# Kernel optimization log

Measured on AMD Instinct MI355X. Metric: run time of the kernel, lower is better.

## Reference

```python
import jax, jax.numpy as jnp
import numpy as np
import math


def _forward(x, f0, theta, sigma, theta0, fbs, mix, w1, b1, w2, b2, conv_w):
    B, I, H, W = x.shape          # config requires B == I == H (== W here)
    S, O, _ = f0.shape            # config requires O == 1
    # ---- log-Gabor filter bank, fully vectorized over (scale, out, in) ----
    yy = jnp.linspace(-1.0, 1.0, H)[:, None]   # meshgrid 'ij': y along rows
    xx = jnp.linspace(-1.0, 1.0, W)[None, :]
    r = jnp.sqrt(xx ** 2 + yy ** 2 + 1e-6)     # [H,W]
    phi = jnp.arctan2(yy, xx)                  # [H,W]
    lr = jnp.log(r)
    log_gabor = jnp.exp(-(lr - jnp.log(f0)[..., None, None]) ** 2
                        / (2.0 * jnp.log(sigma)[..., None, None] ** 2))
    angular = jnp.exp(-(phi - theta[..., None, None]) ** 2
                      / (2.0 * theta0[..., None, None] ** 2))
    filters = log_gabor * angular              # [S,O,I,H,W]
    # ---- FFT (torch fftshift default shifts ALL dims; jnp matches) ----
    xs = jnp.fft.fftshift(jnp.fft.fft2(x))     # [B,I,H,W] complex64
    # ---- frequency attention (two 1x1 convs + softmax over scales) ----
    h1 = jax.nn.relu(jnp.einsum('bchw,oc->bohw', jnp.abs(xs), w1)
                     + b1[None, :, None, None])
    aw = jax.nn.softmax(jnp.einsum('bchw,sc->bshw', h1, w2)
                        + b2[None, :, None, None], axis=1)   # [B,S,H,W]
    # ---- attention-weighted combine. Faithful to torch broadcasting with
    # O==1 and B==I: attended[0,b,i,h,w] = sum_s xs[b,i]*F[s,0,i]*aw[i,s] ----
    attended = jnp.einsum('bihw,sihw,ishw->bihw', xs, filters[:, 0], aw)[None]
    # ---- dynamic frequency band mask (torch slices dims 2,3 = (Cin,H)) ----
    s_idx = jnp.floor((fbs[0, :, 0] + 1.0) / 2.0 * H).astype(jnp.int32)  # [I]
    e_idx = jnp.floor((fbs[0, :, 1] + 1.0) / 2.0 * H).astype(jnp.int32)
    arI = jnp.arange(I)
    arH = jnp.arange(H)
    mk = (arI[None, :] >= s_idx[:, None]) & (arI[None, :] < e_idx[:, None])  # [J,I]
    mh = (arH[None, :] >= s_idx[:, None]) & (arH[None, :] < e_idx[:, None])  # [J,H]
    mask = (mk[:, :, None] & mh[:, None, :]).astype(x.dtype)                 # [J,I,H]
    attended = attended * mask[None, :, :, :, None]
    # ---- back to spatial domain ----
    x_filtered = jnp.fft.ifft2(jnp.fft.ifftshift(attended)).real  # [1,B,I,H,W]
    # ---- spatial 3x3 conv path ----
    x_spatial = jax.lax.conv_general_dilated(
        x, conv_w, window_strides=(1, 1), padding=((1, 1), (1, 1)),
        dimension_numbers=('NCHW', 'OIHW', 'NCHW'))               # [B,1,H,W]
    return mix * x_filtered + (1.0 - mix) * x_spatial[None]


def setup_inputs() -> dict:
    key = jax.random.key(0)
    ks = jax.random.split(key, 10)
    B = I = H = W = 64
    O, S, HID = 1, 3, 64
    PI = math.pi
    x = jax.random.normal(ks[0], (B, I, H, W), dtype=jnp.float32)
    f0 = jnp.ones((S, O, I), jnp.float32)
    theta0 = jnp.ones((S, O, I), jnp.float32)
    sigma = jax.random.uniform(ks[1], (S, O, I), jnp.float32) * PI
    theta = jax.random.uniform(ks[2], (S, O, I), jnp.float32) * PI
    fbs = jax.random.uniform(ks[3], (O, I, 2), jnp.float32)
    mix = jax.random.uniform(ks[4], (1,), jnp.float32)
    w1 = jax.random.normal(ks[5], (HID, I), jnp.float32) * 0.05
    b1 = jnp.zeros((HID,), jnp.float32)
    w2 = jax.random.normal(ks[6], (S, HID), jnp.float32) * 0.05
    b2 = jnp.zeros((S,), jnp.float32)
    conv_w = jax.random.normal(ks[7], (O, I, 3, 3), jnp.float32) / math.sqrt(I * 9)
    return {'x': x, 'f0': f0, 'theta': theta, 'sigma': sigma, 'theta0': theta0,
            'fbs': fbs, 'mix': mix, 'w1': w1, 'b1': b1, 'w2': w2, 'b2': b2,
            'conv_w': conv_w}


def reference(x, f0, theta, sigma, theta0, fbs, mix, w1, b1, w2, b2, conv_w):
    return _forward(x, f0, theta, sigma, theta0, fbs, mix, w1, b1, w2, b2, conv_w)
```

## Files before the change

kernel.cpp:

```cpp
#include <hip/hip_runtime.h>

#define PI_D 3.14159265358979323846

namespace {
constexpr float CT[33] = {
  1.0000000000f,  0.9951847267f,  0.9807852804f,  0.9569403357f,
  0.9238795325f,  0.8819212643f,  0.8314696123f,  0.7730104534f,
  0.7071067812f,  0.6343932842f,  0.5555702330f,  0.4713967368f,
  0.3826834324f,  0.2902846773f,  0.1950903220f,  0.0980171403f,
  0.0f,          -0.0980171403f, -0.1950903220f, -0.2902846773f,
 -0.3826834324f, -0.4713967368f, -0.5555702330f, -0.6343932842f,
 -0.7071067812f, -0.7730104534f, -0.8314696123f, -0.8819212643f,
 -0.9238795325f, -0.9569403357f, -0.9807852804f, -0.9951847267f,
 -1.0f};
constexpr float STb[33] = {
  0.0f,           0.0980171403f,  0.1950903220f,  0.2902846773f,
  0.3826834324f,  0.4713967368f,  0.5555702330f,  0.6343932842f,
  0.7071067812f,  0.7730104534f,  0.8314696123f,  0.8819212643f,
  0.9238795325f,  0.9569403357f,  0.9807852804f,  0.9951847267f,
  1.0f,           0.9951847267f,  0.9807852804f,  0.9569403357f,
  0.9238795325f,  0.8819212643f,  0.8314696123f,  0.7730104534f,
  0.7071067812f,  0.6343932842f,  0.5555702330f,  0.4713967368f,
  0.3826834324f,  0.2902846773f,  0.1950903220f,  0.0980171403f,
  0.0f};
}

__device__ __forceinline__ void bitrev64(float v[64]) {
#pragma unroll
  for (int i = 0; i < 64; ++i) {
    const int j = (int)(__brev((unsigned)i) >> 26);
    if (j > i) { const float tv = v[i]; v[i] = v[j]; v[j] = tv; }
  }
}

template <bool INV, bool REAL>
__device__ __forceinline__ void fft64_stages(float re[64], float im[64]) {
#pragma unroll
  for (int s = 0; s < 6; ++s) {
    const int half = 1 << s;
    const int m = half << 1;
    const int tstep = 32 >> s;
#pragma unroll
    for (int k = 0; k < 64; k += m) {
#pragma unroll
      for (int j = 0; j < half; ++j) {
        const int ti = j * tstep;
        const int a = k + j, b = k + j + half;
        if (REAL && j == 0) {
          const float tr = re[b];
          re[b] = re[a] - tr;
          re[a] = re[a] + tr;
        } else if (REAL && ti == 16) {
          const float t0 = re[b];
          re[b] = re[a];
          im[b] = t0;
          im[a] = -t0;
        } else {
          float tr, tii;
          if (ti == 0) {
            tr = re[b]; tii = im[b];
          } else if (ti == 16) {
            if (INV) { tr = -im[b]; tii = re[b]; }
            else     { tr =  im[b]; tii = -re[b]; }
          } else {
            const float wr = CT[ti];
            const float wi = INV ? STb[ti] : -STb[ti];
            tr  = re[b] * wr - im[b] * wi;
            tii = re[b] * wi + im[b] * wr;
          }
          re[b] = re[a] - tr;  im[b] = im[a] - tii;
          re[a] = re[a] + tr;  im[a] = im[a] + tii;
        }
      }
    }
  }
}

template <bool INV>
__device__ __forceinline__ void fft64_regs(float re[64], float im[64]) {
  bitrev64(re);
  bitrev64(im);
  fft64_stages<INV, false>(re, im);
}

__device__ __forceinline__ void fft64_fwd_real(float re[64], float im[64]) {
  bitrev64(re);
  fft64_stages<false, true>(re, im);
}

__device__ __forceinline__ void band_from_fbs(const float* __restrict__ fbs,
                                              int c, int& s0, int& e0) {
  s0 = (int)floorf((fbs[2 * c]     + 1.0f) * 0.5f * 64.0f);
  e0 = (int)floorf((fbs[2 * c + 1] + 1.0f) * 0.5f * 64.0f);
}

__global__ __launch_bounds__(64) void k_fft_fwd(const float* __restrict__ x,
                                                float* __restrict__ Mag,
                                                float* __restrict__ Fc,
                                                const float* __restrict__ fbs,
                                                const float* __restrict__ w1,
                                                float* __restrict__ w1T) {
  __shared__ float buf[64][65];
  const int t = threadIdx.x;
  const int img = blockIdx.x;
  if (img == 0) {
    for (int k = 0; k < 64; ++k) w1T[t * 64 + k] = w1[k * 64 + t];
  }
  const float* xp = x + ((size_t)img << 12);
  const float4* xr4 = reinterpret_cast<const float4*>(xp + (t << 6));
  float re[64], im[64];
#pragma unroll
  for (int q = 0; q < 16; ++q) {
    const float4 v = xr4[q];
    re[4 * q]     = v.x; re[4 * q + 1] = v.y;
    re[4 * q + 2] = v.z; re[4 * q + 3] = v.w;
  }
#pragma unroll
  for (int j = 0; j < 64; ++j) im[j] = 0.0f;
  fft64_fwd_real(re, im);
#pragma unroll
  for (int j = 0; j < 64; ++j) buf[t][j] = re[j];
  __syncthreads();
#pragma unroll
  for (int j = 0; j < 64; ++j) re[j] = buf[j][t];
  __syncthreads();
#pragma unroll
  for (int j = 0; j < 64; ++j) buf[t][j] = im[j];
  __syncthreads();
#pragma unroll
  for (int j = 0; j < 64; ++j) im[j] = buf[j][t];
  fft64_regs<false>(re, im);
  float* Mg = Mag + ((size_t)img << 12);
#pragma unroll
  for (int j = 0; j < 64; ++j)
    Mg[j * 64 + t] = sqrtf(re[j] * re[j] + im[j] * im[j]);
  const int b = img >> 6, i = img & 63;
  const int b_s = (b + 32) & 63, i_s = (i + 32) & 63;
  int s0, e0;
  band_from_fbs(fbs, b_s, s0, e0);
  if ((i_s >= s0) && (i_s < e0)) {
    float* Fre = Fc + ((size_t)((b << 5) + i) << 13);
    float* Fim = Fre + 4096;
#pragma unroll
    for (int j = 0; j < 64; ++j) {
      Fre[j * 64 + t] = re[j];
      Fim[j * 64 + t] = im[j];
    }
  }
}

__global__ __launch_bounds__(256, 4) void k_attn_conv(
    const float* __restrict__ Mag, const float* __restrict__ w1T,
    const float* __restrict__ b1, const float* __restrict__ w2,
    const float* __restrict__ b2, const float* __restrict__ f0,
    const float* __restrict__ theta, const float* __restrict__ sigma,
    const float* __restrict__ theta0, const float* __restrict__ fbs,
    float* __restrict__ Wc,
    const float* __restrict__ x, const float* __restrict__ cw,
    const float* __restrict__ mixp, float* __restrict__ xsp,
    float* __restrict__ out) {
  __shared__ __align__(16) float sm[64][68];
  __shared__ float part[4][3][64];
  const int t = threadIdx.x;
  const unsigned blk = blockIdx.x;
  const unsigned q5 = blk / 5u;
  const unsigned r5 = blk - q5 * 5u;

  if (r5 == 4u) {
    const int lane = t & 63;
    const int cwv = t >> 6;
    const int b = (int)(q5 >> 4);
    const int row = (int)((q5 & 15u) << 2) | cwv;
    const float* xb = x + ((size_t)b << 18);
    const int rm = row > 0 ? row - 1 : 0;
    const int rp = row < 63 ? row + 1 : 63;
    float P00 = 0.f, P01 = 0.f, P02 = 0.f;
    float P10 = 0.f, P11 = 0.f, P12 = 0.f;
    float P20 = 0.f, P21 = 0.f, P22 = 0.f;
#pragma unroll 4
    for (int ch = 0; ch < 64; ++ch) {
      const float* xc = xb + (ch << 12);
      const float v0 = xc[(rm << 6) + lane];
      const float v1 = xc[(row << 6) + lane];
      const float v2 = xc[(rp << 6) + lane];
      const float* wp = cw + ch * 9;
      P00 = fmaf(v0, wp[0], P00);
      P01 = fmaf(v0, wp[1], P01);
      P02 = fmaf(v0, wp[2], P02);
      P10 = fmaf(v1, wp[3], P10);
      P11 = fmaf(v1, wp[4], P11);
      P12 = fmaf(v1, wp[5], P12);
      P20 = fmaf(v2, wp[6], P20);
      P21 = fmaf(v2, wp[7], P21);
      P22 = fmaf(v2, wp[8], P22);
    }
    const float tmask = (row > 0) ? 1.0f : 0.0f;
    const float bmask = (row < 63) ? 1.0f : 0.0f;
    const float Ql = tmask * P00 + P10 + bmask * P20;
    const float Qm = tmask * P01 + P11 + bmask * P21;
    const float Qr = tmask * P02 + P12 + bmask * P22;
    const float fromL = __shfl_up(Ql, 1, 64);
    const float fromR = __shfl_down(Qr, 1, 64);
    float acc = Qm;
    if (lane > 0) acc += fromL;
    if (lane < 63) acc += fromR;
    xsp[((size_t)b << 12) + (row << 6) + lane] = acc;
    const int b_s = (b + 32) & 63;
    int s0, e0;
    band_from_fbs(fbs, b_s, s0, e0);
    const float val = (1.0f - mixp[0]) * acc;
    float* ob = out + ((size_t)b << 18) + (row << 6) + lane;
#pragma unroll 4
    for (int i2 = 0; i2 < 64; ++i2) {
      const int i_s = (i2 + 32) & 63;
      if (!(i_s >= s0 && i_s < e0)) ob[(size_t)i2 << 12] = val;
    }
    return;
  }

  const int ai = (int)(4u * q5 + r5);
  const int i = ai >> 6;
  const int h = ai & 63;
  const int b_f = (i + 32) & 63;
  const int u_f = (h + 32) & 63;
  {
    const int ct = t >> 2;
    const int m4 = t & 3;
    const float4* src = reinterpret_cast<const float4*>(
        Mag + ((((size_t)(b_f << 6)) + (ct ^ 32)) << 12) + (u_f << 6) + m4 * 16);
    float4* dst = reinterpret_cast<float4*>(&sm[ct][(m4 ^ 2) * 16]);
    dst[0] = src[0];
    dst[1] = src[1];
    dst[2] = src[2];
    dst[3] = src[3];
  }
  __syncthreads();
  const int lane = t & 63;
  const int wv = __builtin_amdgcn_readfirstlane(t >> 6);
  const int k0 = wv << 4;
  float acc[16];
#pragma unroll
  for (int k = 0; k < 16; ++k) acc[k] = 0.0f;
#pragma unroll
  for (int c = 0; c < 64; ++c) {
    const float mc = sm[c][lane];
    const float* wrow = w1T + (c << 6) + k0;
#pragma unroll
    for (int k = 0; k < 16; ++k) acc[k] = fmaf(wrow[k], mc, acc[k]);
  }
  float p0 = 0.0f, p1 = 0.0f, p2 = 0.0f;
#pragma unroll
  for (int k = 0; k < 16; ++k) {
    const float hv = fmaxf(acc[k] + b1[k0 + k], 0.0f);
    p0 = fmaf(w2[k0 + k], hv, p0);
    p1 = fmaf(w2[64 + k0 + k], hv, p1);
    p2 = fmaf(w2[128 + k0 + k], hv, p2);
  }
  if (wv != 0) {
    part[wv][0][lane] = p0;
    part[wv][1][lane] = p1;
    part[wv][2][lane] = p2;
  }
  __syncthreads();
  if (wv != 0) return;
  float l0 = b2[0] + p0 + part[1][0][lane] + part[2][0][lane] + part[3][0][lane];
  float l1 = b2[1] + p1 + part[1][1][lane] + part[2][1][lane] + part[3][1][lane];
  float l2 = b2[2] + p2 + part[1][2][lane] + part[2][2][lane] + part[3][2][lane];
  float mx = fmaxf(l0, fmaxf(l1, l2));
  float e0v = expf(l0 - mx), e1 = expf(l1 - mx), e2 = expf(l2 - mx);
  float inv = 1.0f / (e0v + e1 + e2);
  float aw0 = e0v * inv, aw1 = e1 * inv, aw2 = e2 * inv;
  const float yy = -1.0f + (float)h * (2.0f / 63.0f);
  const float xx = -1.0f + (float)lane * (2.0f / 63.0f);
  const float r = sqrtf(xx * xx + yy * yy + 1e-6f);
  const float lr = logf(r);
  const float phi = atan2f(yy, xx);
  float wc = 0.0f;
  const float aws[3] = {aw0, aw1, aw2};
#pragma unroll
  for (int s = 0; s < 3; ++s) {
    const float f0v = f0[s * 64 + i];
    const float sgv = sigma[s * 64 + i];
    const float thv = theta[s * 64 + i];
    const float t0v = theta0[s * 64 + i];
    const float ls = logf(sgv);
    const float d1 = lr - logf(f0v);
    const float g1 = expf(-(d1 * d1) / (2.0f * ls * ls));
    const float d2 = phi - thv;
    const float g2 = expf(-(d2 * d2) / (2.0f * t0v * t0v));
    wc = fmaf(g1 * g2, aws[s], wc);
  }
  Wc[((i << 6) + h) * 64 + lane] = wc;
}

__global__ __launch_bounds__(64) void k_ifft_act(
    const float* __restrict__ Fc, const float* __restrict__ Wc,
    const float* __restrict__ xsp, const float* __restrict__ fbs,
    const float* __restrict__ mixp, float* __restrict__ out) {
  const int b = blockIdx.x >> 5;
  const int i = blockIdx.x & 31;
  const int b_s = (b + 32) & 63, i_s = i + 32;
  int s0, e0;
  band_from_fbs(fbs, b_s, s0, e0);
  if (!((i_s >= s0) && (i_s < e0))) return;
  __shared__ float buf[64][65];
  const int t = threadIdx.x;
  const float* Fre = Fc + ((size_t)((b << 5) + i) << 13);
  const float* Fim = Fre + 4096;
  const float* Wcp = Wc + ((size_t)i_s << 12);
  const int u_s = (t + 32) & 63;
  const float rmask = (u_s >= s0 && u_s < e0) ? 1.0f : 0.0f;
  const float* wrow = Wcp + (u_s << 6);
  const float4* fr4 = reinterpret_cast<const float4*>(Fre + (t << 6));
  const float4* fi4 = reinterpret_cast<const float4*>(Fim + (t << 6));
  float re[64], im[64];
#pragma unroll
  for (int q = 0; q < 16; ++q) {
    const int j0 = 4 * q;
    const float4 w4 = *reinterpret_cast<const float4*>(wrow + ((j0 + 32) & 63));
    const float4 vr = fr4[q];
    const float4 vi = fi4[q];
    const float w0 = rmask * w4.x, w1v = rmask * w4.y;
    const float w2v = rmask * w4.z, w3v = rmask * w4.w;
    re[j0]     = vr.x * w0;  re[j0 + 1] = vr.y * w1v;
    re[j0 + 2] = vr.z * w2v; re[j0 + 3] = vr.w * w3v;
    im[j0]     = vi.x * w0;  im[j0 + 1] = vi.y * w1v;
    im[j0 + 2] = vi.z * w2v; im[j0 + 3] = vi.w * w3v;
  }
  fft64_regs<true>(re, im);
#pragma unroll
  for (int j = 0; j < 64; ++j) buf[t][j] = re[j];
  __syncthreads();
#pragma unroll
  for (int j = 0; j < 64; ++j) re[j] = buf[j][t];
  __syncthreads();
#pragma unroll
  for (int j = 0; j < 64; ++j) buf[t][j] = im[j];
  __syncthreads();
#pragma unroll
  for (int j = 0; j < 64; ++j) im[j] = buf[j][t];
  fft64_regs<true>(re, im);
  const float mixv = mixp[0];
  const float sc = mixv * (1.0f / 4096.0f);
  const float om = 1.0f - mixv;
  float* op = out + (((size_t)(b << 6) + i) << 12);
  const float* xp = xsp + ((size_t)b << 12);
#pragma unroll
  for (int j = 0; j < 64; ++j)
    op[j * 64 + t] = fmaf(sc, re[j], om * xp[j * 64 + t]);
}

extern "C" void kernel_launch(void* const* d_in, const int* in_sizes, int n_in,
                              void* d_out, int out_size, void* d_ws, size_t ws_size,
                              hipStream_t stream) {
  const float* x      = (const float*)d_in[0];
  const float* f0     = (const float*)d_in[1];
  const float* theta  = (const float*)d_in[2];
  const float* sigma  = (const float*)d_in[3];
  const float* theta0 = (const float*)d_in[4];
  const float* fbs    = (const float*)d_in[5];
  const float* mix    = (const float*)d_in[6];
  const float* w1     = (const float*)d_in[7];
  const float* b1     = (const float*)d_in[8];
  const float* w2     = (const float*)d_in[9];
  const float* b2     = (const float*)d_in[10];
  const float* cw     = (const float*)d_in[11];
  float* out = (float*)d_out;
  char* ws = (char*)d_ws;
  float* Mag = (float*)(ws);
  float* Fc  = (float*)(ws + 67108864);
  float* Wc  = (float*)(ws + 134217728);
  float* xsp = (float*)(ws + 134217728 + 1048576);
  float* w1T = (float*)(ws + 134217728 + 2097152);

  k_fft_fwd<<<4096, 64, 0, stream>>>(x, Mag, Fc, fbs, w1, w1T);
  k_attn_conv<<<5120, 256, 0, stream>>>(Mag, w1T, b1, w2, b2, f0, theta, sigma,
                                        theta0, fbs, Wc, x, cw, mix, xsp, out);
  k_ifft_act<<<2048, 64, 0, stream>>>(Fc, Wc, xsp, fbs, mix, out);
}
```

Before: 213.4 us.

## Exploit FFT magnitude conjugate symmetry to halve attention work and Mag stores

Real-input FFT magnitudes are symmetric, so the forward kernel now stores only half the Mag rows and the attention kernel computes attention for 32 rows per image. Mirrored attention weights are recovered by a lane shuffle. The shared-memory staging is dropped in favour of direct strided global reads, and the iFFT skips loading weight rows for inactive bands. The risk is that uncoalesced strided Mag loads and the symmetry bookkeeping (rows 0/32 edge cases) are slower or subtly wrong.

Measured after the change: 189.5 us. 1.13x faster.

```diff
diff --git a/kernel.cpp b/kernel.cpp
--- a/kernel.cpp
+++ b/kernel.cpp
@@ -131,8 +131,9 @@
   for (int j = 0; j < 64; ++j) im[j] = buf[j][t];
   fft64_regs<false>(re, im);
   float* Mg = Mag + ((size_t)img << 12);
-#pragma unroll
-  for (int j = 0; j < 64; ++j)
+  Mg[t] = sqrtf(re[0] * re[0] + im[0] * im[0]);
+#pragma unroll
+  for (int j = 33; j < 64; ++j)
     Mg[j * 64 + t] = sqrtf(re[j] * re[j] + im[j] * im[j]);
   const int b = img >> 6, i = img & 63;
   const int b_s = (b + 32) & 63, i_s = (i + 32) & 63;
@@ -159,18 +160,17 @@
     const float* __restrict__ x, const float* __restrict__ cw,
     const float* __restrict__ mixp, float* __restrict__ xsp,
     float* __restrict__ out) {
-  __shared__ __align__(16) float sm[64][68];
   __shared__ float part[4][3][64];
   const int t = threadIdx.x;
   const unsigned blk = blockIdx.x;
-  const unsigned q5 = blk / 5u;
-  const unsigned r5 = blk - q5 * 5u;
-
-  if (r5 == 4u) {
+  const unsigned q3 = blk / 3u;
+  const unsigned r3 = blk - q3 * 3u;
+
+  if (r3 == 2u) {
     const int lane = t & 63;
     const int cwv = t >> 6;
-    const int b = (int)(q5 >> 4);
-    const int row = (int)((q5 & 15u) << 2) | cwv;
+    const int b = (int)(q3 >> 4);
+    const int row = (int)((q3 & 15u) << 2) | cwv;
     const float* xb = x + ((size_t)b << 18);
     const int rm = row > 0 ? row - 1 : 0;
     const int rp = row < 63 ? row + 1 : 63;
@@ -218,32 +218,23 @@
     return;
   }
 
-  const int ai = (int)(4u * q5 + r5);
-  const int i = ai >> 6;
-  const int h = ai & 63;
-  const int b_f = (i + 32) & 63;
-  const int u_f = (h + 32) & 63;
-  {
-    const int ct = t >> 2;
-    const int m4 = t & 3;
-    const float4* src = reinterpret_cast<const float4*>(
-        Mag + ((((size_t)(b_f << 6)) + (ct ^ 32)) << 12) + (u_f << 6) + m4 * 16);
-    float4* dst = reinterpret_cast<float4*>(&sm[ct][(m4 ^ 2) * 16]);
-    dst[0] = src[0];
-    dst[1] = src[1];
-    dst[2] = src[2];
-    dst[3] = src[3];
-  }
-  __syncthreads();
+  const int ai = (int)(2u * q3 + r3);
   const int lane = t & 63;
   const int wv = __builtin_amdgcn_readfirstlane(t >> 6);
   const int k0 = wv << 4;
+  const int i = ai >> 5;
+  const int h = (ai & 31) + 1;
+  const int b_f = (i + 32) & 63;
+  const int u_f = (h + 32) & 63;
+  const int v_f = (lane + 32) & 63;
+  const int pos_f = (u_f << 6) + v_f;
+  const float* Mb = Mag + (((size_t)(b_f << 6)) << 12) + pos_f;
   float acc[16];
 #pragma unroll
   for (int k = 0; k < 16; ++k) acc[k] = 0.0f;
-#pragma unroll
+#pragma unroll 4
   for (int c = 0; c < 64; ++c) {
-    const float mc = sm[c][lane];
+    const float mc = Mb[(size_t)((c + 32) & 63) << 12];
     const float* wrow = w1T + (c << 6) + k0;
 #pragma unroll
     for (int k = 0; k < 16; ++k) acc[k] = fmaf(wrow[k], mc, acc[k]);
@@ -270,7 +261,15 @@
   float e0v = expf(l0 - mx), e1 = expf(l1 - mx), e2 = expf(l2 - mx);
   float inv = 1.0f / (e0v + e1 + e2);
   float aw0 = e0v * inv, aw1 = e1 * inv, aw2 = e2 * inv;
-  const float yy = -1.0f + (float)h * (2.0f / 63.0f);
+  int hw = h;
+  if (h != 32) {
+    const int src = (64 - lane) & 63;
+    aw0 = __shfl(aw0, src, 64);
+    aw1 = __shfl(aw1, src, 64);
+    aw2 = __shfl(aw2, src, 64);
+    hw = 64 - h;
+  }
+  const float yy = -1.0f + (float)hw * (2.0f / 63.0f);
   const float xx = -1.0f + (float)lane * (2.0f / 63.0f);
   const float r = sqrtf(xx * xx + yy * yy + 1e-6f);
   const float lr = logf(r);
@@ -290,7 +289,7 @@
     const float g2 = expf(-(d2 * d2) / (2.0f * t0v * t0v));
     wc = fmaf(g1 * g2, aws[s], wc);
   }
-  Wc[((i << 6) + h) * 64 + lane] = wc;
+  Wc[((i << 6) + hw) * 64 + lane] = wc;
 }
 
 __global__ __launch_bounds__(64) void k_ifft_act(
@@ -309,7 +308,7 @@
   const float* Fim = Fre + 4096;
   const float* Wcp = Wc + ((size_t)i_s << 12);
   const int u_s = (t + 32) & 63;
-  const float rmask = (u_s >= s0 && u_s < e0) ? 1.0f : 0.0f;
+  const bool act_row = (u_s >= s0 && u_s < e0);
   const float* wrow = Wcp + (u_s << 6);
   const float4* fr4 = reinterpret_cast<const float4*>(Fre + (t << 6));
   const float4* fi4 = reinterpret_cast<const float4*>(Fim + (t << 6));
@@ -317,15 +316,15 @@
 #pragma unroll
   for (int q = 0; q < 16; ++q) {
     const int j0 = 4 * q;
-    const float4 w4 = *reinterpret_cast<const float4*>(wrow + ((j0 + 32) & 63));
+    const float4 w4 = act_row
+        ? *reinterpret_cast<const float4*>(wrow + ((j0 + 32) & 63))
+        : make_float4(0.0f, 0.0f, 0.0f, 0.0f);
     const float4 vr = fr4[q];
     const float4 vi = fi4[q];
-    const float w0 = rmask * w4.x, w1v = rmask * w4.y;
-    const float w2v = rmask * w4.z, w3v = rmask * w4.w;
-    re[j0]     = vr.x * w0;  re[j0 + 1] = vr.y * w1v;
-    re[j0 + 2] = vr.z * w2v; re[j0 + 3] = vr.w * w3v;
-    im[j0]     = vi.x * w0;  im[j0 + 1] = vi.y * w1v;
-    im[j0 + 2] = vi.z * w2v; im[j0 + 3] = vi.w * w3v;
+    re[j0]     = vr.x * w4.x;  re[j0 + 1] = vr.y * w4.y;
+    re[j0 + 2] = vr.z * w4.z;  re[j0 + 3] = vr.w * w4.w;
+    im[j0]     = vi.x * w4.x;  im[j0 + 1] = vi.y * w4.y;
+    im[j0 + 2] = vi.z * w4.z;  im[j0 + 3] = vi.w * w4.w;
   }
   fft64_regs<true>(re, im);
 #pragma unroll
@@ -374,7 +373,7 @@
   float* w1T = (float*)(ws + 134217728 + 2097152);
 
   k_fft_fwd<<<4096, 64, 0, stream>>>(x, Mag, Fc, fbs, w1, w1T);
-  k_attn_conv<<<5120, 256, 0, stream>>>(Mag, w1T, b1, w2, b2, f0, theta, sigma,
+  k_attn_conv<<<3072, 256, 0, stream>>>(Mag, w1T, b1, w2, b2, f0, theta, sigma,
                                         theta0, fbs, Wc, x, cw, mix, xsp, out);
   k_ifft_act<<<2048, 64, 0, stream>>>(Fc, Wc, xsp, fbs, mix, out);
 }
```
